# Kernel tuning notes

Hardware: AMD Instinct MI355X
Metric: run time of the kernel (lower is better)

The kernel has to match this reference:

```python
import jax, jax.numpy as jnp
import numpy as np

N_EMBD = 1024
N_HEAD = 16
HEAD_DIM = N_EMBD // N_HEAD
NEG = -1e9


def setup_inputs() -> dict:
    key = jax.random.key(0)
    ks = jax.random.split(key, 5)
    B, S = 2, 2048
    x = jax.random.normal(ks[0], (B, S, N_EMBD), dtype=jnp.float32)
    # qkv_proj: Linear(n_embd, 3*n_embd) -> weight used as x @ W_qkv (W stored [in, out])
    scale = 1.0 / np.sqrt(N_EMBD)
    W_qkv = jax.random.normal(ks[1], (N_EMBD, 3 * N_EMBD), dtype=jnp.float32) * scale
    b_qkv = jax.random.normal(ks[2], (3 * N_EMBD,), dtype=jnp.float32) * 0.02
    W_out = jax.random.normal(ks[3], (N_EMBD, N_EMBD), dtype=jnp.float32) * scale
    b_out = jax.random.normal(ks[4], (N_EMBD,), dtype=jnp.float32) * 0.02
    return {"x": x, "W_qkv": W_qkv, "b_qkv": b_qkv, "W_out": W_out, "b_out": b_out}


def reference(x, W_qkv, b_qkv, W_out, b_out):
    B, S, E = x.shape
    qkv = x @ W_qkv + b_qkv                      # [B,S,3E]
    q, k, v = jnp.split(qkv, 3, axis=-1)
    # [B,S,E] -> [B,H,S,D]
    def split_heads(t):
        return t.reshape(B, S, N_HEAD, HEAD_DIM).transpose(0, 2, 1, 3)
    q, k, v = split_heads(q), split_heads(k), split_heads(v)
    scores = jnp.einsum("bhqd,bhkd->bhqk", q, k) / jnp.sqrt(jnp.float32(HEAD_DIM))
    causal = jnp.tril(jnp.ones((S, S), dtype=bool))
    scores = jnp.where(causal, scores, NEG)
    attn = jax.nn.softmax(scores, axis=-1)
    out = jnp.einsum("bhqk,bhkd->bhqd", attn, v)  # [B,H,S,D]
    out = out.transpose(0, 2, 1, 3).reshape(B, S, E)
    return out @ W_out + b_out
```

## Files before the change

### kernel.cpp

```cpp
#include <hip/hip_runtime.h>
#include <hip/hip_bf16.h>

#define BATCH 2
#define SEQ   2048
#define EMBD  1024
#define NHEAD 16
#define HDIM  64
#define QKV3  (3 * EMBD)

typedef __attribute__((ext_vector_type(8))) __bf16 bf16x8;
typedef __attribute__((ext_vector_type(4))) __bf16 bf16x4;
typedef __attribute__((ext_vector_type(4))) float f32x4;

#define QSCALE 0.18033688011112043f

__global__ __launch_bounds__(256) void cast_f32_bf16(
    const float* __restrict__ in, __bf16* __restrict__ out)
{
    int i = (blockIdx.x * 256 + threadIdx.x) * 8;
    float4 a = *(const float4*)&in[i];
    float4 b = *(const float4*)&in[i + 4];
    bf16x8 o;
    o[0] = (__bf16)a.x; o[1] = (__bf16)a.y; o[2] = (__bf16)a.z; o[3] = (__bf16)a.w;
    o[4] = (__bf16)b.x; o[5] = (__bf16)b.y; o[6] = (__bf16)b.z; o[7] = (__bf16)b.w;
    *(bf16x8*)&out[i] = o;
}

__global__ __launch_bounds__(256) void transpose_cast_bf16(
    const float* __restrict__ in, __bf16* __restrict__ out, int K, int N)
{
    __shared__ float t[64][65];
    const int k0 = blockIdx.y * 64, n0 = blockIdx.x * 64;
    const int tid = threadIdx.x;
    #pragma unroll
    for (int p = 0; p < 4; p++) {
        int kr = p * 16 + (tid >> 4);
        int c4 = (tid & 15) * 4;
        float4 v = *(const float4*)&in[(size_t)(k0 + kr) * N + n0 + c4];
        t[kr][c4] = v.x; t[kr][c4 + 1] = v.y; t[kr][c4 + 2] = v.z; t[kr][c4 + 3] = v.w;
    }
    __syncthreads();
    #pragma unroll
    for (int p = 0; p < 4; p++) {
        int nr = p * 16 + (tid >> 4);
        int k4 = (tid & 15) * 4;
        bf16x4 o;
        o[0] = (__bf16)t[k4 + 0][nr];
        o[1] = (__bf16)t[k4 + 1][nr];
        o[2] = (__bf16)t[k4 + 2][nr];
        o[3] = (__bf16)t[k4 + 3][nr];
        *(bf16x4*)&out[(size_t)(n0 + nr) * K + k0 + k4] = o;
    }
}

__global__ __launch_bounds__(256) void gemm_qkv_mfma(
    const __bf16* __restrict__ A,
    const __bf16* __restrict__ Bt,
    const float* __restrict__ bias,
    __bf16* __restrict__ qh, __bf16* __restrict__ kh, __bf16* __restrict__ vt)
{
    const int N = QKV3, K = EMBD;
    __shared__ __align__(16) __bf16 As[128 * 32];
    __shared__ __align__(16) __bf16 Bs[128 * 32];

    const int tid  = threadIdx.x;
    const int lane = tid & 63;
    const int wave = tid >> 6;
    const int wm = (wave >> 1) * 64;
    const int wn = (wave & 1) * 64;
    const int m0 = blockIdx.y * 128;
    const int n0 = blockIdx.x * 128;
    const int lm = lane & 15;
    const int kq = lane >> 4;

    f32x4 acc[4][4] = {};

    for (int k0 = 0; k0 < K; k0 += 32) {
        __syncthreads();
        #pragma unroll
        for (int r = 0; r < 2; r++) {
            int flat = r * 256 + tid;
            int row  = flat >> 2;
            int off  = (flat & 3) * 16;
            const char* ga = (const char*)(A + (size_t)(m0 + row) * K + k0) + off;
            char* la = (char*)As + flat * 16;
            __builtin_amdgcn_global_load_lds(
                (const __attribute__((address_space(1))) void*)ga,
                (__attribute__((address_space(3))) void*)la, 16, 0, 0);
            const char* gb = (const char*)(Bt + (size_t)(n0 + row) * K + k0) + off;
            char* lb = (char*)Bs + flat * 16;
            __builtin_amdgcn_global_load_lds(
                (const __attribute__((address_space(1))) void*)gb,
                (__attribute__((address_space(3))) void*)lb, 16, 0, 0);
        }
        __syncthreads();

        bf16x8 af[4], bf[4];
        #pragma unroll
        for (int t = 0; t < 4; t++) {
            af[t] = *(const bf16x8*)&As[(wm + t * 16 + lm) * 32 + kq * 8];
            bf[t] = *(const bf16x8*)&Bs[(wn + t * 16 + lm) * 32 + kq * 8];
        }
        #pragma unroll
        for (int i = 0; i < 4; i++)
            #pragma unroll
            for (int j = 0; j < 4; j++)
                acc[i][j] = __builtin_amdgcn_mfma_f32_16x16x32_bf16(
                    af[i], bf[j], acc[i][j], 0, 0, 0);
    }

    const int r0 = kq * 4;
    #pragma unroll
    for (int i = 0; i < 4; i++) {
        const int row0 = m0 + wm + i * 16 + r0;
        const int b  = row0 >> 11;
        const int s0 = row0 & 2047;
        #pragma unroll
        for (int j = 0; j < 4; j++) {
            const int col = n0 + wn + j * 16 + lm;
            const float bv = bias[col];
            const int region = col >> 10;
            const int hh = (col >> 6) & 15;
            const int dd = col & 63;
            const size_t bh = (size_t)(b * 16 + hh);
            if (region == 2) {
                bf16x4 o;
                #pragma unroll
                for (int r = 0; r < 4; r++) o[r] = (__bf16)(acc[i][j][r] + bv);
                *(bf16x4*)&vt[(bh * 64 + dd) * SEQ + s0] = o;
            } else {
                __bf16* dst = (region == 0) ? qh : kh;
                const float sc = (region == 0) ? QSCALE : 1.0f;
                #pragma unroll
                for (int r = 0; r < 4; r++)
                    dst[(bh * SEQ + s0 + r) * 64 + dd] = (__bf16)((acc[i][j][r] + bv) * sc);
            }
        }
    }
}

__global__ __launch_bounds__(256) void gemm_bt_mfma_f32out(
    const __bf16* __restrict__ A,
    const __bf16* __restrict__ Bt,
    const float* __restrict__ bias,
    float* __restrict__ C,
    int M, int N, int K)
{
    __shared__ __align__(16) __bf16 As[128 * 32];
    __shared__ __align__(16) __bf16 Bs[128 * 32];

    const int tid  = threadIdx.x;
    const int lane = tid & 63;
    const int wave = tid >> 6;
    const int wm = (wave >> 1) * 64;
    const int wn = (wave & 1) * 64;
    const int m0 = blockIdx.y * 128;
    const int n0 = blockIdx.x * 128;
    const int lm = lane & 15;
    const int kq = lane >> 4;

    f32x4 acc[4][4] = {};

    for (int k0 = 0; k0 < K; k0 += 32) {
        __syncthreads();
        #pragma unroll
        for (int r = 0; r < 2; r++) {
            int flat = r * 256 + tid;
            int row  = flat >> 2;
            int off  = (flat & 3) * 16;
            const char* ga = (const char*)(A + (size_t)(m0 + row) * K + k0) + off;
            char* la = (char*)As + flat * 16;
            __builtin_amdgcn_global_load_lds(
                (const __attribute__((address_space(1))) void*)ga,
                (__attribute__((address_space(3))) void*)la, 16, 0, 0);
            const char* gb = (const char*)(Bt + (size_t)(n0 + row) * K + k0) + off;
            char* lb = (char*)Bs + flat * 16;
            __builtin_amdgcn_global_load_lds(
                (const __attribute__((address_space(1))) void*)gb,
                (__attribute__((address_space(3))) void*)lb, 16, 0, 0);
        }
        __syncthreads();

        bf16x8 af[4], bf[4];
        #pragma unroll
        for (int t = 0; t < 4; t++) {
            af[t] = *(const bf16x8*)&As[(wm + t * 16 + lm) * 32 + kq * 8];
            bf[t] = *(const bf16x8*)&Bs[(wn + t * 16 + lm) * 32 + kq * 8];
        }
        #pragma unroll
        for (int i = 0; i < 4; i++)
            #pragma unroll
            for (int j = 0; j < 4; j++)
                acc[i][j] = __builtin_amdgcn_mfma_f32_16x16x32_bf16(
                    af[i], bf[j], acc[i][j], 0, 0, 0);
    }

    const int r0 = kq * 4;
    #pragma unroll
    for (int i = 0; i < 4; i++) {
        #pragma unroll
        for (int j = 0; j < 4; j++) {
            int col = n0 + wn + j * 16 + lm;
            float bv = bias[col];
            #pragma unroll
            for (int r = 0; r < 4; r++) {
                int row = m0 + wm + i * 16 + r0 + r;
                C[(size_t)row * N + col] = acc[i][j][r] + bv;
            }
        }
    }
}

__global__ __launch_bounds__(256, 3) void attn_kpar_mfma(
    const __bf16* __restrict__ qh, const __bf16* __restrict__ kh,
    const __bf16* __restrict__ vt, __bf16* __restrict__ attn)
{
    __shared__ __align__(16) char smem[16896];

    const int tid  = threadIdx.x;
    const int wave = tid >> 6;
    const int lane = tid & 63;
    const int quad = lane >> 4;
    const int c    = lane & 15;

    const int bh = blockIdx.x;
    const int b  = bh >> 4;
    const int h  = bh & 15;
    const int qblk = (int)(gridDim.y - 1) - blockIdx.y;
    const int q0 = qblk * 32;

    const int hoff = h * HDIM;
    const __bf16* qbase = qh + (size_t)bh * SEQ * 64;
    const __bf16* kbase = kh + (size_t)bh * SEQ * 64;
    const __bf16* vbase = vt + (size_t)bh * 64 * SEQ;

    bf16x8 aq[2][2];
    #pragma unroll
    for (int qf = 0; qf < 2; qf++) {
        const __bf16* qrow = qbase + (size_t)(q0 + qf * 16 + c) * 64 + quad * 8;
        aq[qf][0] = *(const bf16x8*)(qrow);
        aq[qf][1] = *(const bf16x8*)(qrow + 32);
    }

    f32x4 acc[2][4] = {};
    float lpart[2][4] = {};

    char* pbw = smem + wave * 4096;
    const int ntiles = q0 / 64 + 1;

    for (int t = wave; t < ntiles; t += 4) {
        const int k0 = t * 64;
        const bool diag = (t == ntiles - 1);

        bf16x8 bk[4][2];
        #pragma unroll
        for (int jj = 0; jj < 4; jj++) {
            const __bf16* krow = kbase + (size_t)(k0 + jj * 16 + c) * 64 + quad * 8;
            bk[jj][0] = *(const bf16x8*)(krow);
            bk[jj][1] = *(const bf16x8*)(krow + 32);
        }
        bf16x8 bv[4][2];
        #pragma unroll
        for (int dd = 0; dd < 4; dd++) {
            const __bf16* vr = vbase + (size_t)(dd * 16 + c) * SEQ + k0 + quad * 8;
            bv[dd][0] = *(const bf16x8*)(vr);
            bv[dd][1] = *(const bf16x8*)(vr + 32);
        }

        #pragma unroll
        for (int jj = 0; jj < 4; jj++) {
            const int col = jj * 16 + c;
            const int kabs_c = k0 + col;
            const int ab = (col >> 5) * 1024 + ((col >> 3) & 3) * 256 + (col & 7) * 2;
            #pragma unroll
            for (int qf = 0; qf < 2; qf++) {
                f32x4 s = {};
                s = __builtin_amdgcn_mfma_f32_16x16x32_bf16(aq[qf][0], bk[jj][0], s, 0, 0, 0);
                s = __builtin_amdgcn_mfma_f32_16x16x32_bf16(aq[qf][1], bk[jj][1], s, 0, 0, 0);
                char* pq = pbw + qf * 2048 + ab;
                const int qabs0 = q0 + qf * 16 + quad * 4;
                #pragma unroll
                for (int r = 0; r < 4; r++) {
                    float p;
                    if (diag && (kabs_c > qabs0 + r)) p = 0.f;
                    else p = __builtin_amdgcn_exp2f(s[r]);
                    lpart[qf][r] += p;
                    *(__bf16*)(pq + (quad * 4 + r) * 16) = (__bf16)p;
                }
            }
        }

        bf16x8 ap[2][2];
        #pragma unroll
        for (int qf = 0; qf < 2; qf++) {
            ap[qf][0] = *(const bf16x8*)(pbw + qf * 2048 + lane * 16);
            ap[qf][1] = *(const bf16x8*)(pbw + qf * 2048 + 1024 + lane * 16);
        }

        #pragma unroll
        for (int dd = 0; dd < 4; dd++) {
            #pragma unroll
            for (int qf = 0; qf < 2; qf++) {
                acc[qf][dd] = __builtin_amdgcn_mfma_f32_16x16x32_bf16(ap[qf][0], bv[dd][0], acc[qf][dd], 0, 0, 0);
                acc[qf][dd] = __builtin_amdgcn_mfma_f32_16x16x32_bf16(ap[qf][1], bv[dd][1], acc[qf][dd], 0, 0, 0);
            }
        }
    }

    #pragma unroll
    for (int qf = 0; qf < 2; qf++)
        #pragma unroll
        for (int r = 0; r < 4; r++) {
            float v = lpart[qf][r];
            v += __shfl_xor(v, 1);
            v += __shfl_xor(v, 2);
            v += __shfl_xor(v, 4);
            v += __shfl_xor(v, 8);
            lpart[qf][r] = v;
        }

    __syncthreads();

    float* Ored = (float*)smem;
    float* lred = (float*)(smem + 16640);

    if (wave < 2) {
        float* R = Ored + wave * (32 * 65);
        #pragma unroll
        for (int qf = 0; qf < 2; qf++)
            #pragma unroll
            for (int dd = 0; dd < 4; dd++)
                #pragma unroll
                for (int r = 0; r < 4; r++)
                    R[(qf * 16 + quad * 4 + r) * 65 + dd * 16 + c] = acc[qf][dd][r];
        if (c == 0) {
            #pragma unroll
            for (int qf = 0; qf < 2; qf++)
                #pragma unroll
                for (int r = 0; r < 4; r++)
                    lred[wave * 32 + qf * 16 + quad * 4 + r] = lpart[qf][r];
        }
    }
    __syncthreads();
    if (wave >= 2) {
        float* R = Ored + (wave - 2) * (32 * 65);
        #pragma unroll
        for (int qf = 0; qf < 2; qf++)
            #pragma unroll
            for (int dd = 0; dd < 4; dd++)
                #pragma unroll
                for (int r = 0; r < 4; r++)
                    R[(qf * 16 + quad * 4 + r) * 65 + dd * 16 + c] += acc[qf][dd][r];
        if (c == 0) {
            #pragma unroll
            for (int qf = 0; qf < 2; qf++)
                #pragma unroll
                for (int r = 0; r < 4; r++)
                    lred[(wave - 2) * 32 + qf * 16 + quad * 4 + r] += lpart[qf][r];
        }
    }
    __syncthreads();

    {
        const int row = tid >> 3;
        const int cg  = tid & 7;
        const float l = lred[row] + lred[32 + row];
        const float inv = 1.f / l;
        const float* R0 = Ored + row * 65 + cg * 8;
        const float* R1 = R0 + 32 * 65;
        bf16x8 o;
        #pragma unroll
        for (int i = 0; i < 8; i++) o[i] = (__bf16)((R0[i] + R1[i]) * inv);
        *(bf16x8*)&attn[((size_t)b * SEQ + q0 + row) * EMBD + hoff + cg * 8] = o;
    }
}

extern "C" void kernel_launch(void* const* d_in, const int* in_sizes, int n_in,
                              void* d_out, int out_size, void* d_ws, size_t ws_size,
                              hipStream_t stream)
{
    const float* x     = (const float*)d_in[0];
    const float* W_qkv = (const float*)d_in[1];
    const float* b_qkv = (const float*)d_in[2];
    const float* W_out = (const float*)d_in[3];
    const float* b_out = (const float*)d_in[4];
    float* out = (float*)d_out;

    const int M = BATCH * SEQ;

    __bf16* xbf    = (__bf16*)d_ws;
    __bf16* Wqkv_t = xbf    + (size_t)M * EMBD;
    __bf16* Wout_t = Wqkv_t + (size_t)QKV3 * EMBD;
    __bf16* qh     = Wout_t + (size_t)EMBD * EMBD;
    __bf16* kh     = qh     + (size_t)M * EMBD;
    __bf16* vtbuf  = kh     + (size_t)M * EMBD;
    __bf16* attn   = vtbuf  + (size_t)M * EMBD;

    cast_f32_bf16<<<(M * EMBD) / (256 * 8), 256, 0, stream>>>(x, xbf);
    {
        dim3 g(QKV3 / 64, EMBD / 64);
        transpose_cast_bf16<<<g, 256, 0, stream>>>(W_qkv, Wqkv_t, EMBD, QKV3);
    }
    {
        dim3 g(EMBD / 64, EMBD / 64);
        transpose_cast_bf16<<<g, 256, 0, stream>>>(W_out, Wout_t, EMBD, EMBD);
    }
    {
        dim3 grid(QKV3 / 128, M / 128);
        gemm_qkv_mfma<<<grid, 256, 0, stream>>>(xbf, Wqkv_t, b_qkv, qh, kh, vtbuf);
    }
    {
        dim3 grid(BATCH * NHEAD, SEQ / 32);
        attn_kpar_mfma<<<grid, 256, 0, stream>>>(qh, kh, vtbuf, attn);
    }
    {
        dim3 grid(EMBD / 128, M / 128);
        gemm_bt_mfma_f32out<<<grid, 256, 0, stream>>>(attn, Wout_t, b_out, out, M, EMBD, EMBD);
    }
}
```

Before: 220.1 us.

## Keep softmax probabilities in registers by computing transposed scores and 16x16x16 PV MFMAs

Swaps the operand order of the QK^T MFMA so each lane holds four consecutive keys for one query, which matches the B-operand layout of a 16x16x16 bf16 MFMA. The P tile then feeds the PV product straight from registers, removing the per-wave LDS write and read round trip for probabilities. V is loaded in 4-element chunks, and the row-sum reduction and output write indexing are changed to the transposed layout. In exchange it issues twice as many smaller MFMAs for PV and uses narrower V loads.

```diff
diff --git a/kernel.cpp b/kernel.cpp
--- a/kernel.cpp
+++ b/kernel.cpp
@@ -11,8 +11,20 @@
 typedef __attribute__((ext_vector_type(8))) __bf16 bf16x8;
 typedef __attribute__((ext_vector_type(4))) __bf16 bf16x4;
 typedef __attribute__((ext_vector_type(4))) float f32x4;
+typedef __attribute__((ext_vector_type(4))) short short4v;
 
 #define QSCALE 0.18033688011112043f
+
+static __device__ __forceinline__ f32x4 mfma_16x16x16_bf16(
+    short4v a, short4v b, f32x4 c)
+{
+#if __has_builtin(__builtin_amdgcn_mfma_f32_16x16x16_bf16)
+    return __builtin_amdgcn_mfma_f32_16x16x16_bf16(
+        __builtin_bit_cast(bf16x4, a), __builtin_bit_cast(bf16x4, b), c, 0, 0, 0);
+#else
+    return __builtin_amdgcn_mfma_f32_16x16x16bf16_1k(a, b, c, 0, 0, 0);
+#endif
+}
 
 __global__ __launch_bounds__(256) void cast_f32_bf16(
     const float* __restrict__ in, __bf16* __restrict__ out)
@@ -243,9 +255,8 @@
     }
 
     f32x4 acc[2][4] = {};
-    float lpart[2][4] = {};
-
-    char* pbw = smem + wave * 4096;
+    float lpart[2] = {};
+
     const int ntiles = q0 / 64 + 1;
 
     for (int t = wave; t < ntiles; t += 4) {
@@ -259,65 +270,49 @@
             bk[jj][0] = *(const bf16x8*)(krow);
             bk[jj][1] = *(const bf16x8*)(krow + 32);
         }
-        bf16x8 bv[4][2];
+        short4v av[4][4];
         #pragma unroll
         for (int dd = 0; dd < 4; dd++) {
-            const __bf16* vr = vbase + (size_t)(dd * 16 + c) * SEQ + k0 + quad * 8;
-            bv[dd][0] = *(const bf16x8*)(vr);
-            bv[dd][1] = *(const bf16x8*)(vr + 32);
+            const __bf16* vr = vbase + (size_t)(dd * 16 + c) * SEQ + k0 + quad * 4;
+            #pragma unroll
+            for (int jj = 0; jj < 4; jj++)
+                av[dd][jj] = *(const short4v*)(vr + jj * 16);
         }
 
         #pragma unroll
         for (int jj = 0; jj < 4; jj++) {
-            const int col = jj * 16 + c;
-            const int kabs_c = k0 + col;
-            const int ab = (col >> 5) * 1024 + ((col >> 3) & 3) * 256 + (col & 7) * 2;
+            const int key0 = k0 + jj * 16 + quad * 4;
             #pragma unroll
             for (int qf = 0; qf < 2; qf++) {
                 f32x4 s = {};
-                s = __builtin_amdgcn_mfma_f32_16x16x32_bf16(aq[qf][0], bk[jj][0], s, 0, 0, 0);
-                s = __builtin_amdgcn_mfma_f32_16x16x32_bf16(aq[qf][1], bk[jj][1], s, 0, 0, 0);
-                char* pq = pbw + qf * 2048 + ab;
-                const int qabs0 = q0 + qf * 16 + quad * 4;
+                s = __builtin_amdgcn_mfma_f32_16x16x32_bf16(bk[jj][0], aq[qf][0], s, 0, 0, 0);
+                s = __builtin_amdgcn_mfma_f32_16x16x32_bf16(bk[jj][1], aq[qf][1], s, 0, 0, 0);
+
+                const int qabs = q0 + qf * 16 + c;
+                short4v pb;
                 #pragma unroll
                 for (int r = 0; r < 4; r++) {
                     float p;
-                    if (diag && (kabs_c > qabs0 + r)) p = 0.f;
+                    if (diag && (key0 + r > qabs)) p = 0.f;
                     else p = __builtin_amdgcn_exp2f(s[r]);
-                    lpart[qf][r] += p;
-                    *(__bf16*)(pq + (quad * 4 + r) * 16) = (__bf16)p;
+                    lpart[qf] += p;
+                    __bf16 pv = (__bf16)p;
+                    pb[r] = __builtin_bit_cast(short, pv);
                 }
+                #pragma unroll
+                for (int dd = 0; dd < 4; dd++)
+                    acc[qf][dd] = mfma_16x16x16_bf16(av[dd][jj], pb, acc[qf][dd]);
             }
         }
-
-        bf16x8 ap[2][2];
-        #pragma unroll
-        for (int qf = 0; qf < 2; qf++) {
-            ap[qf][0] = *(const bf16x8*)(pbw + qf * 2048 + lane * 16);
-            ap[qf][1] = *(const bf16x8*)(pbw + qf * 2048 + 1024 + lane * 16);
-        }
-
-        #pragma unroll
-        for (int dd = 0; dd < 4; dd++) {
-            #pragma unroll
-            for (int qf = 0; qf < 2; qf++) {
-                acc[qf][dd] = __builtin_amdgcn_mfma_f32_16x16x32_bf16(ap[qf][0], bv[dd][0], acc[qf][dd], 0, 0, 0);
-                acc[qf][dd] = __builtin_amdgcn_mfma_f32_16x16x32_bf16(ap[qf][1], bv[dd][1], acc[qf][dd], 0, 0, 0);
-            }
-        }
-    }
-
-    #pragma unroll
-    for (int qf = 0; qf < 2; qf++)
-        #pragma unroll
-        for (int r = 0; r < 4; r++) {
-            float v = lpart[qf][r];
-            v += __shfl_xor(v, 1);
-            v += __shfl_xor(v, 2);
-            v += __shfl_xor(v, 4);
-            v += __shfl_xor(v, 8);
-            lpart[qf][r] = v;
-        }
+    }
+
+    #pragma unroll
+    for (int qf = 0; qf < 2; qf++) {
+        float v = lpart[qf];
+        v += __shfl_xor(v, 16);
+        v += __shfl_xor(v, 32);
+        lpart[qf] = v;
+    }
 
     __syncthreads();
 
@@ -332,13 +327,11 @@
             for (int dd = 0; dd < 4; dd++)
                 #pragma unroll
                 for (int r = 0; r < 4; r++)
-                    R[(qf * 16 + quad * 4 + r) * 65 + dd * 16 + c] = acc[qf][dd][r];
-        if (c == 0) {
+                    R[(qf * 16 + c) * 65 + dd * 16 + quad * 4 + r] = acc[qf][dd][r];
+        if (quad == 0) {
             #pragma unroll
             for (int qf = 0; qf < 2; qf++)
-                #pragma unroll
-                for (int r = 0; r < 4; r++)
-                    lred[wave * 32 + qf * 16 + quad * 4 + r] = lpart[qf][r];
+                lred[wave * 32 + qf * 16 + c] = lpart[qf];
         }
     }
     __syncthreads();
@@ -350,13 +343,11 @@
             for (int dd = 0; dd < 4; dd++)
                 #pragma unroll
                 for (int r = 0; r < 4; r++)
-                    R[(qf * 16 + quad * 4 + r) * 65 + dd * 16 + c] += acc[qf][dd][r];
-        if (c == 0) {
+                    R[(qf * 16 + c) * 65 + dd * 16 + quad * 4 + r] += acc[qf][dd][r];
+        if (quad == 0) {
             #pragma unroll
             for (int qf = 0; qf < 2; qf++)
-                #pragma unroll
-                for (int r = 0; r < 4; r++)
-                    lred[(wave - 2) * 32 + qf * 16 + quad * 4 + r] += lpart[qf][r];
+                lred[(wave - 2) * 32 + qf * 16 + c] += lpart[qf];
         }
     }
     __syncthreads();
```

New measurement: 243.2 us. 1.1x slower.
